# Performance work log

Measured on AMD Instinct MI355X. Metric: run time of the kernel, lower is better.

The kernel has to match this reference:

```python
import jax, jax.numpy as jnp
import numpy as np

B, S = 1024, 256
E, EU = 8, 1            # total experts, universal experts
ES = E - EU             # specialized experts
UW = 0.3                # universal_expert_weight
NSTEPS = 1001
COV = 512
H = 128
DATA_DIM = 2


def setup_inputs() -> dict:
    key = jax.random.key(0)
    ks = iter(jax.random.split(key, 64))

    def nrm(shape, s=0.02):
        return jax.random.normal(next(ks), shape, jnp.float32) * s

    inp = {
        "y_t": jax.random.normal(next(ks), (B, S, 1), jnp.float32),
        "y_0_hat": jax.random.normal(next(ks), (B, S, 1), jnp.float32),
        "cov_embedding": jax.random.normal(next(ks), (B, COV), jnp.float32),
        "t": jax.random.randint(next(ks), (B,), 0, NSTEPS),
    }
    for l, nin in zip((1, 2, 3), (DATA_DIM, H, H)):
        inp[f"l{l}_emb"] = jax.random.uniform(next(ks), (NSTEPS, H), jnp.float32)  # embed.weight.uniform_()
        inp[f"l{l}_W"] = nrm((E, nin, H))      # per-expert Linear weights
        inp[f"l{l}_b"] = jnp.zeros((E, H), jnp.float32)
        inp[f"l{l}_Wc"] = nrm((COV, H))        # cov_projection
        inp[f"l{l}_bc"] = jnp.zeros((H,), jnp.float32)
        inp[f"l{l}_Wr1"] = nrm((COV, COV // 2))  # specialized_router layer 1
        inp[f"l{l}_br1"] = jnp.zeros((COV // 2,), jnp.float32)
        inp[f"l{l}_Wr2"] = nrm((COV // 2, ES))   # specialized_router layer 2
        inp[f"l{l}_br2"] = jnp.zeros((ES,), jnp.float32)
    inp["W4"] = nrm((H, 1))
    inp["b4"] = jnp.zeros((1,), jnp.float32)
    return inp


def _moe_layer(x, t, cov, emb, W, b, Wc, bc, Wr1, br1, Wr2, br2):
    # x: [B,S,in]; t: [B] int; cov: [B,COV]
    gamma = emb[t][:, None, :]                                   # [B,1,H]
    hr = jax.nn.relu(cov @ Wr1 + br1)                            # router (dropout inactive in eval)
    rw = jax.nn.softmax(hr @ Wr2 + br2, axis=-1) * (1.0 - UW)    # [B,ES] specialized routing weights
    w = jnp.concatenate(
        [jnp.full((x.shape[0], EU), UW / EU, x.dtype), rw], axis=1
    )                                                            # [B,E] full routing weights
    # gamma factors out of the weighted sum over experts, so fuse expert GEMMs + weighting:
    mix = jnp.einsum('bsi,eio,be->bso', x, W, w) + jnp.einsum('be,eo->bo', w, b)[:, None, :]
    mix = gamma * mix
    cov_gamma = cov @ Wc + bc                                    # [B,H]
    mix = mix * (1.0 + cov_gamma[:, None, :])
    usage = rw.mean(axis=0)                                      # mean over batch
    load = jnp.mean((usage - 1.0 / ES) ** 2)                     # mse vs uniform
    return mix, load


def reference(y_t, y_0_hat, cov_embedding, t,
              l1_emb, l1_W, l1_b, l1_Wc, l1_bc, l1_Wr1, l1_br1, l1_Wr2, l1_br2,
              l2_emb, l2_W, l2_b, l2_Wc, l2_bc, l2_Wr1, l2_br1, l2_Wr2, l2_br2,
              l3_emb, l3_W, l3_b, l3_Wc, l3_bc, l3_Wr1, l3_br1, l3_Wr2, l3_br2,
              W4, b4):
    h = jnp.concatenate([y_t, y_0_hat], axis=-1)                 # cat_y_pred: [B,S,2]
    h, ld1 = _moe_layer(h, t, cov_embedding, l1_emb, l1_W, l1_b, l1_Wc, l1_bc, l1_Wr1, l1_br1, l1_Wr2, l1_br2)
    h = jax.nn.softplus(h)
    h, ld2 = _moe_layer(h, t, cov_embedding, l2_emb, l2_W, l2_b, l2_Wc, l2_bc, l2_Wr1, l2_br1, l2_Wr2, l2_br2)
    h = jax.nn.softplus(h)
    h, ld3 = _moe_layer(h, t, cov_embedding, l3_emb, l3_W, l3_b, l3_Wc, l3_bc, l3_Wr1, l3_br1, l3_Wr2, l3_br2)
    h = jax.nn.softplus(h)
    out = h @ W4 + b4                                            # [B,S,1] velocity
    return out, ld1 + ld2 + ld3
```

## Files before the change

### kernel.cpp

```cpp
#include <hip/hip_runtime.h>
#include <hip/hip_bf16.h>
#include <math.h>

#define B_    1024
#define S_    256
#define COV_  512
#define H_    128
#define E_    8
#define ES_   7

#define W_WS_OFF   0
#define COVG_OFF   24576
#define USAGE_OFF  417792

#define AT_STRIDE  136
#define WT_STRIDE  40

typedef __attribute__((ext_vector_type(8))) short bf16x8;
typedef __attribute__((ext_vector_type(4))) float f32x4;

__device__ __forceinline__ float softplus_f(float x) {
    return fmaxf(x, 0.0f) + __logf(1.0f + __expf(-fabsf(x)));
}

__device__ __forceinline__ unsigned pk2_bf16(float a, float b) {
    __hip_bfloat162 h = __float22bfloat162_rn(make_float2(a, b));
    return *reinterpret_cast<unsigned*>(&h);
}
__device__ __forceinline__ void split_pair(float a, float b, unsigned &hi, unsigned &lo) {
    hi = pk2_bf16(a, b);
    float ha = __uint_as_float(hi << 16);
    float hb = __uint_as_float(hi & 0xffff0000u);
    lo = pk2_bf16(a - ha, b - hb);
}

struct RouterArgs {
    const float* cov;
    const float* Wr1[3];
    const float* br1[3];
    const float* Wr2[3];
    const float* br2[3];
    const float* Wc[3];
    const float* bc[3];
    float* ws;
};

__global__ __launch_bounds__(768) void router_kernel(RouterArgs a) {
    const int l   = blockIdx.y;
    const int b0  = blockIdx.x * 8;
    const int tid = threadIdx.x;

    __shared__ float4 covs[8][COV_ / 4];
    __shared__ float  part[4][3072];
    __shared__ float  hr[8][256];
    __shared__ float  susage[ES_];
    if (tid < ES_) susage[tid] = 0.0f;

    for (int f = tid; f < 1024; f += 768) {
        const int bb = f >> 7, k4 = f & 127;
        covs[bb][k4] = ((const float4*)(a.cov + (size_t)(b0 + bb) * COV_))[k4];
    }
    __syncthreads();

    {
        const int cp = tid % 192;
        const int ks = tid / 192;
        const int c0 = cp * 2;
        const float* __restrict__ Wp; int rs;
        if (c0 < 256) { Wp = a.Wr1[l] + c0;         rs = 256; }
        else          { Wp = a.Wc[l]  + (c0 - 256); rs = 128; }

        float acc0[8], acc1[8];
        #pragma unroll
        for (int bb = 0; bb < 8; ++bb) { acc0[bb] = 0.f; acc1[bb] = 0.f; }

        const int k4beg = ks * 32, k4end = k4beg + 32;
        #pragma unroll 2
        for (int k4 = k4beg; k4 < k4end; ++k4) {
            float2 w0 = *(const float2*)(Wp + (size_t)(4 * k4 + 0) * rs);
            float2 w1 = *(const float2*)(Wp + (size_t)(4 * k4 + 1) * rs);
            float2 w2 = *(const float2*)(Wp + (size_t)(4 * k4 + 2) * rs);
            float2 w3 = *(const float2*)(Wp + (size_t)(4 * k4 + 3) * rs);
            #pragma unroll
            for (int bb = 0; bb < 8; ++bb) {
                float4 cv = covs[bb][k4];
                acc0[bb] = fmaf(cv.x, w0.x, acc0[bb]);
                acc1[bb] = fmaf(cv.x, w0.y, acc1[bb]);
                acc0[bb] = fmaf(cv.y, w1.x, acc0[bb]);
                acc1[bb] = fmaf(cv.y, w1.y, acc1[bb]);
                acc0[bb] = fmaf(cv.z, w2.x, acc0[bb]);
                acc1[bb] = fmaf(cv.z, w2.y, acc1[bb]);
                acc0[bb] = fmaf(cv.w, w3.x, acc0[bb]);
                acc1[bb] = fmaf(cv.w, w3.y, acc1[bb]);
            }
        }
        #pragma unroll
        for (int bb = 0; bb < 8; ++bb)
            *(float2*)&part[ks][bb * 384 + c0] = make_float2(acc0[bb], acc1[bb]);
    }
    __syncthreads();

    {
        const int p0 = tid * 4;
        float4 s = {0.f, 0.f, 0.f, 0.f};
        #pragma unroll
        for (int ks = 0; ks < 4; ++ks) {
            float4 v = *(const float4*)&part[ks][p0];
            s.x += v.x; s.y += v.y; s.z += v.z; s.w += v.w;
        }
        const int bb = p0 / 384;
        const int c  = p0 % 384;
        const float sv[4] = {s.x, s.y, s.z, s.w};
        if (c < 256) {
            #pragma unroll
            for (int q = 0; q < 4; ++q)
                hr[bb][c + q] = fmaxf(sv[q] + a.br1[l][c + q], 0.0f);
        } else {
            #pragma unroll
            for (int q = 0; q < 4; ++q)
                a.ws[COVG_OFF + (size_t)(l * B_ + b0 + bb) * H_ + (c - 256 + q)] = sv[q] + a.bc[l][c - 256 + q];
        }
    }
    __syncthreads();

    {
        const int wave = tid >> 6;
        const int lane = tid & 63;
        if (wave < 8) {
            const int bb = wave;
            const int o = lane >> 3;
            const int g = lane & 7;
            float p = 0.0f;
            if (o < ES_) {
                #pragma unroll
                for (int m = 0; m < 32; ++m) {
                    const int k = g * 32 + m;
                    p = fmaf(hr[bb][k], a.Wr2[l][k * ES_ + o], p);
                }
            }
            p += __shfl_xor(p, 1);
            p += __shfl_xor(p, 2);
            p += __shfl_xor(p, 4);
            const float lg = p + ((o < ES_) ? a.br2[l][o] : 0.0f);
            float v[ES_];
            #pragma unroll
            for (int oo = 0; oo < ES_; ++oo) v[oo] = __shfl(lg, oo * 8, 64);
            if (lane == 0) {
                const int b = b0 + bb;
                float mx = v[0];
                #pragma unroll
                for (int oo = 1; oo < ES_; ++oo) mx = fmaxf(mx, v[oo]);
                float ex[ES_]; float s = 0.0f;
                #pragma unroll
                for (int oo = 0; oo < ES_; ++oo) { ex[oo] = __expf(v[oo] - mx); s += ex[oo]; }
                const float inv = 0.7f / s;
                float* wout = a.ws + W_WS_OFF + (size_t)(l * B_ + b) * 8;
                wout[0] = 0.3f;
                #pragma unroll
                for (int oo = 0; oo < ES_; ++oo) {
                    const float rwv = ex[oo] * inv;
                    wout[1 + oo] = rwv;
                    atomicAdd(&susage[oo], rwv);
                }
            }
        }
    }
    __syncthreads();
    if (tid < ES_) atomicAdd(a.ws + USAGE_OFF + l * ES_ + tid, susage[tid]);
}

struct MainArgs {
    const float* y_t;
    const float* y0;
    const int*   t;
    const float* emb[3];
    const float* W1;
    const float* W2;
    const float* W3;
    const float* b_[3];
    const float* W4;
    const float* b4;
    float* ws;
    float* out;
};

__global__ __launch_bounds__(1024, 4) void main_kernel(MainArgs a) {
    __shared__ unsigned short Ahi[256 * AT_STRIDE];
    __shared__ unsigned short Alo[256 * AT_STRIDE];
    __shared__ unsigned short WtBuf[2][128 * WT_STRIDE];
    __shared__ float GPs[2][128];
    __shared__ float GPBs[2][128];
    __shared__ float W4s[128];

    const int tid  = threadIdx.x;
    const int b    = blockIdx.x;
    const int lane = tid & 63;
    const int w    = tid >> 6;
    const int wm   = w >> 1;
    const int wn   = w & 1;
    const int nl   = lane & 15;
    const int quad = lane >> 4;
    const int tb   = a.t[b];

    float* L1f = (float*)WtBuf;

    if (tid < 384) {
        const int l = tid >> 7, j = tid & 127;
        const float* wv = a.ws + W_WS_OFF + (size_t)(l * B_ + b) * 8;
        const float gamma = a.emb[l][tb * H_ + j];
        const float covg  = a.ws[COVG_OFF + (size_t)(l * B_ + b) * H_ + j];
        const float gp = gamma * (1.0f + covg);
        const float* bl = a.b_[l];
        float bm = 0.0f;
        #pragma unroll
        for (int e = 0; e < E_; ++e) bm = fmaf(wv[e], bl[e * H_ + j], bm);
        if (l == 0) {
            float s0 = 0.0f, s1 = 0.0f;
            #pragma unroll
            for (int e = 0; e < E_; ++e) {
                s0 = fmaf(wv[e], a.W1[e * 256 + j], s0);
                s1 = fmaf(wv[e], a.W1[e * 256 + 128 + j], s1);
            }
            L1f[j]       = gp * s0;
            L1f[128 + j] = gp * s1;
            L1f[256 + j] = gp * bm;
        } else {
            GPs[l - 1][j]  = gp;
            GPBs[l - 1][j] = gp * bm;
        }
    }
    if (tid < 128) W4s[tid] = a.W4[tid];
    __syncthreads();

    {
        const int tok = tid >> 2;
        const int jh  = (tid & 3) * 32;
        const float x0 = a.y_t[b * S_ + tok];
        const float x1 = a.y0[b * S_ + tok];
        #pragma unroll
        for (int g = 0; g < 4; ++g) {
            const int jb = jh + g * 8;
            unsigned hp[4], lp[4];
            #pragma unroll
            for (int p = 0; p < 4; ++p) {
                const int j0 = jb + 2 * p;
                float m0 = fmaf(x0, L1f[j0],     fmaf(x1, L1f[128 + j0],     L1f[256 + j0]));
                float m1 = fmaf(x0, L1f[j0 + 1], fmaf(x1, L1f[128 + j0 + 1], L1f[256 + j0 + 1]));
                split_pair(softplus_f(m0), softplus_f(m1), hp[p], lp[p]);
            }
            *(uint4*)&Ahi[tok * AT_STRIDE + jb] = make_uint4(hp[0], hp[1], hp[2], hp[3]);
            *(uint4*)&Alo[tok * AT_STRIDE + jb] = make_uint4(lp[0], lp[1], lp[2], lp[3]);
        }
    }

    const int bj  = tid & 127;
    const int bkg = tid >> 7;

    for (int L = 0; L < 2; ++L) {
        const float* __restrict__ Wg = L ? a.W3 : a.W2;
        const float* wv = a.ws + W_WS_OFF + (size_t)((L + 1) * B_ + b) * 8;
        float we[E_];
        #pragma unroll
        for (int e = 0; e < E_; ++e) we[e] = wv[e];

        f32x4 acc[2][4];
        #pragma unroll
        for (int mt = 0; mt < 2; ++mt)
            #pragma unroll
            for (int nt = 0; nt < 4; ++nt)
                acc[mt][nt] = (f32x4){0.f, 0.f, 0.f, 0.f};

        unsigned bh[2], blo_[2];
        auto build = [&](int kc) {
            float bacc[4] = {0.f, 0.f, 0.f, 0.f};
            const float* base = Wg + (size_t)(kc * 32 + bkg * 4) * H_ + bj;
            #pragma unroll
            for (int e = 0; e < E_; ++e) {
                const float* p = base + (size_t)e * (H_ * H_);
                const float wE = we[e];
                #pragma unroll
                for (int i = 0; i < 4; ++i)
                    bacc[i] = fmaf(wE, p[i * H_], bacc[i]);
            }
            split_pair(bacc[0], bacc[1], bh[0], blo_[0]);
            split_pair(bacc[2], bacc[3], bh[1], blo_[1]);
        };

        build(0);

        for (int kc = 0; kc < 4; ++kc) {
            __syncthreads();
            *(uint2*)&WtBuf[0][bj * WT_STRIDE + bkg * 4] = make_uint2(bh[0], bh[1]);
            *(uint2*)&WtBuf[1][bj * WT_STRIDE + bkg * 4] = make_uint2(blo_[0], blo_[1]);
            __syncthreads();

            const int ka = kc * 32 + quad * 8;
            bf16x8 Af[2], Al[2], Bf[4], Bl[4];
            #pragma unroll
            for (int mt = 0; mt < 2; ++mt) {
                const int row = (wm * 32 + mt * 16 + nl) * AT_STRIDE + ka;
                Af[mt] = *(const bf16x8*)&Ahi[row];
                Al[mt] = *(const bf16x8*)&Alo[row];
            }
            #pragma unroll
            for (int nt = 0; nt < 4; ++nt) {
                const int row = (wn * 64 + nt * 16 + nl) * WT_STRIDE + quad * 8;
                Bf[nt] = *(const bf16x8*)&WtBuf[0][row];
                Bl[nt] = *(const bf16x8*)&WtBuf[1][row];
            }
            #pragma unroll
            for (int mt = 0; mt < 2; ++mt)
                #pragma unroll
                for (int nt = 0; nt < 4; ++nt) {
                    acc[mt][nt] = __builtin_amdgcn_mfma_f32_16x16x32_bf16(Af[mt], Bf[nt], acc[mt][nt], 0, 0, 0);
                    acc[mt][nt] = __builtin_amdgcn_mfma_f32_16x16x32_bf16(Af[mt], Bl[nt], acc[mt][nt], 0, 0, 0);
                    acc[mt][nt] = __builtin_amdgcn_mfma_f32_16x16x32_bf16(Al[mt], Bf[nt], acc[mt][nt], 0, 0, 0);
                }

            if (kc < 3) build(kc + 1);
        }
        __syncthreads();

        if (L == 0) {
            #pragma unroll
            for (int nt = 0; nt < 4; ++nt) {
                const int n = wn * 64 + nt * 16 + nl;
                const float gp = GPs[0][n], gpb = GPBs[0][n];
                #pragma unroll
                for (int mt = 0; mt < 2; ++mt) {
                    const int tok0 = wm * 32 + mt * 16 + quad * 4;
                    #pragma unroll
                    for (int rp = 0; rp < 2; ++rp) {
                        const float h0 = softplus_f(fmaf(gp, acc[mt][nt][2 * rp],     gpb));
                        const float h1 = softplus_f(fmaf(gp, acc[mt][nt][2 * rp + 1], gpb));
                        unsigned hh, ll;
                        split_pair(h0, h1, hh, ll);
                        const int t0 = tok0 + 2 * rp;
                        Ahi[t0 * AT_STRIDE + n]       = (unsigned short)hh;
                        Ahi[(t0 + 1) * AT_STRIDE + n] = (unsigned short)(hh >> 16);
                        Alo[t0 * AT_STRIDE + n]       = (unsigned short)ll;
                        Alo[(t0 + 1) * AT_STRIDE + n] = (unsigned short)(ll >> 16);
                    }
                }
            }
        } else {
            float po[2][4];
            #pragma unroll
            for (int mt = 0; mt < 2; ++mt)
                #pragma unroll
                for (int r = 0; r < 4; ++r) po[mt][r] = 0.0f;
            #pragma unroll
            for (int nt = 0; nt < 4; ++nt) {
                const int n = wn * 64 + nt * 16 + nl;
                const float gp = GPs[1][n], gpb = GPBs[1][n], w4 = W4s[n];
                #pragma unroll
                for (int mt = 0; mt < 2; ++mt)
                    #pragma unroll
                    for (int r = 0; r < 4; ++r) {
                        const float h = softplus_f(fmaf(gp, acc[mt][nt][r], gpb));
                        po[mt][r] = fmaf(h, w4, po[mt][r]);
                    }
            }
            #pragma unroll
            for (int mt = 0; mt < 2; ++mt)
                #pragma unroll
                for (int r = 0; r < 4; ++r) {
                    po[mt][r] += __shfl_xor(po[mt][r], 1);
                    po[mt][r] += __shfl_xor(po[mt][r], 2);
                    po[mt][r] += __shfl_xor(po[mt][r], 4);
                    po[mt][r] += __shfl_xor(po[mt][r], 8);
                }
            float* pos = (float*)WtBuf;
            if (nl == 0) {
                #pragma unroll
                for (int mt = 0; mt < 2; ++mt)
                    #pragma unroll
                    for (int r = 0; r < 4; ++r)
                        pos[(wm * 32 + mt * 16 + quad * 4 + r) * 2 + wn] = po[mt][r];
            }
            __syncthreads();
            if (tid < 256)
                a.out[b * S_ + tid] = pos[2 * tid] + pos[2 * tid + 1] + a.b4[0];
        }
    }

    if (b == 0 && tid == 0) {
        float ld = 0.0f;
        for (int l = 0; l < 3; ++l)
            for (int o = 0; o < ES_; ++o) {
                float u = a.ws[USAGE_OFF + l * ES_ + o] * (1.0f / (float)B_);
                float d = u - (1.0f / (float)ES_);
                ld = fmaf(d, d, ld);
            }
        a.out[B_ * S_] = ld * (1.0f / (float)ES_);
    }
}

extern "C" void kernel_launch(void* const* d_in, const int* in_sizes, int n_in,
                              void* d_out, int out_size, void* d_ws, size_t ws_size,
                              hipStream_t stream) {
    (void)in_sizes; (void)n_in; (void)out_size; (void)ws_size;

    RouterArgs ra;
    ra.cov = (const float*)d_in[2];
    ra.ws  = (float*)d_ws;

    MainArgs ma;
    ma.y_t = (const float*)d_in[0];
    ma.y0  = (const float*)d_in[1];
    ma.t   = (const int*)d_in[3];
    for (int l = 0; l < 3; ++l) {
        const int base = 4 + l * 9;
        ma.emb[l] = (const float*)d_in[base + 0];
        ma.b_[l]  = (const float*)d_in[base + 2];
        ra.Wc[l]  = (const float*)d_in[base + 3];
        ra.bc[l]  = (const float*)d_in[base + 4];
        ra.Wr1[l] = (const float*)d_in[base + 5];
        ra.br1[l] = (const float*)d_in[base + 6];
        ra.Wr2[l] = (const float*)d_in[base + 7];
        ra.br2[l] = (const float*)d_in[base + 8];
    }
    ma.W1 = (const float*)d_in[4 + 0 * 9 + 1];
    ma.W2 = (const float*)d_in[4 + 1 * 9 + 1];
    ma.W3 = (const float*)d_in[4 + 2 * 9 + 1];
    ma.W4 = (const float*)d_in[31];
    ma.b4 = (const float*)d_in[32];
    ma.ws  = (float*)d_ws;
    ma.out = (float*)d_out;

    (void)hipMemsetAsync((char*)d_ws + USAGE_OFF * sizeof(float), 0, 24 * sizeof(float), stream);
    router_kernel<<<dim3(128, 3, 1), 768, 0, stream>>>(ra);
    main_kernel<<<dim3(1024, 1, 1), 1024, 0, stream>>>(ma);
}
```

Measured before the change: 291.4 us.

## Swizzle LDS layout, double-buffer weight tiles, drop memset and usage atomics

Replaces the padded LDS strides with XOR-swizzled layouts for the activation and combined-weight tiles, and double-buffers the weight tile so each k-chunk needs one barrier instead of two. Per-layer gamma, bias and W4 values now live in registers instead of shared memory. The router writes per-block usage partials rather than doing global atomics, so the memset launch goes away and block 0 reduces the partials at kernel start. The trade-off is higher register pressure under a 1024-thread launch bound, plus a serial 128-element reduction in block 0.

```diff
diff --git a/kernel.cpp b/kernel.cpp
--- a/kernel.cpp
+++ b/kernel.cpp
@@ -12,9 +12,6 @@
 #define W_WS_OFF   0
 #define COVG_OFF   24576
 #define USAGE_OFF  417792
-
-#define AT_STRIDE  136
-#define WT_STRIDE  40
 
 typedef __attribute__((ext_vector_type(8))) short bf16x8;
 typedef __attribute__((ext_vector_type(4))) float f32x4;
@@ -166,7 +163,8 @@
         }
     }
     __syncthreads();
-    if (tid < ES_) atomicAdd(a.ws + USAGE_OFF + l * ES_ + tid, susage[tid]);
+    if (tid < ES_)
+        a.ws[USAGE_OFF + (size_t)(l * 128 + blockIdx.x) * 8 + tid] = susage[tid];
 }
 
 struct MainArgs {
@@ -185,12 +183,9 @@
 };
 
 __global__ __launch_bounds__(1024, 4) void main_kernel(MainArgs a) {
-    __shared__ unsigned short Ahi[256 * AT_STRIDE];
-    __shared__ unsigned short Alo[256 * AT_STRIDE];
-    __shared__ unsigned short WtBuf[2][128 * WT_STRIDE];
-    __shared__ float GPs[2][128];
-    __shared__ float GPBs[2][128];
-    __shared__ float W4s[128];
+    __shared__ __align__(16) char smem[163840];
+    unsigned short* Ahi = (unsigned short*)smem;
+    unsigned short* Alo = (unsigned short*)(smem + 65536);
 
     const int tid  = threadIdx.x;
     const int b    = blockIdx.x;
@@ -202,44 +197,77 @@
     const int quad = lane >> 4;
     const int tb   = a.t[b];
 
-    float* L1f = (float*)WtBuf;
-
-    if (tid < 384) {
-        const int l = tid >> 7, j = tid & 127;
-        const float* wv = a.ws + W_WS_OFF + (size_t)(l * B_ + b) * 8;
-        const float gamma = a.emb[l][tb * H_ + j];
-        const float covg  = a.ws[COVG_OFF + (size_t)(l * B_ + b) * H_ + j];
-        const float gp = gamma * (1.0f + covg);
-        const float* bl = a.b_[l];
-        float bm = 0.0f;
-        #pragma unroll
-        for (int e = 0; e < E_; ++e) bm = fmaf(wv[e], bl[e * H_ + j], bm);
-        if (l == 0) {
-            float s0 = 0.0f, s1 = 0.0f;
-            #pragma unroll
-            for (int e = 0; e < E_; ++e) {
-                s0 = fmaf(wv[e], a.W1[e * 256 + j], s0);
-                s1 = fmaf(wv[e], a.W1[e * 256 + 128 + j], s1);
-            }
-            L1f[j]       = gp * s0;
-            L1f[128 + j] = gp * s1;
-            L1f[256 + j] = gp * bm;
-        } else {
-            GPs[l - 1][j]  = gp;
-            GPBs[l - 1][j] = gp * bm;
-        }
-    }
-    if (tid < 128) W4s[tid] = a.W4[tid];
+    if (b == 0 && tid < 64) {
+        float d2 = 0.0f;
+        if (tid < 21) {
+            const int l = tid / 7, o = tid % 7;
+            float s = 0.0f;
+            for (int bx = 0; bx < 128; ++bx)
+                s += a.ws[USAGE_OFF + (size_t)(l * 128 + bx) * 8 + o];
+            const float u = s * (1.0f / (float)B_);
+            const float d = u - (1.0f / (float)ES_);
+            d2 = d * d;
+        }
+        float tot = 0.0f;
+        #pragma unroll
+        for (int i = 0; i < 21; ++i) tot += __shfl(d2, i, 64);
+        if (tid == 0) a.out[B_ * S_] = tot * (1.0f / (float)ES_);
+    }
+
+    float wvL[2][E_];
+    #pragma unroll
+    for (int l = 0; l < 2; ++l) {
+        const float* wv = a.ws + W_WS_OFF + (size_t)((l + 1) * B_ + b) * 8;
+        #pragma unroll
+        for (int e = 0; e < E_; ++e) wvL[l][e] = wv[e];
+    }
+    float gpr[2][4], gpbr[2][4], w4r[4];
+    #pragma unroll
+    for (int l = 0; l < 2; ++l) {
+        const int li = l + 1;
+        #pragma unroll
+        for (int nt = 0; nt < 4; ++nt) {
+            const int n = wn * 64 + nt * 16 + nl;
+            const float covg  = a.ws[COVG_OFF + (size_t)(li * B_ + b) * H_ + n];
+            const float gamma = a.emb[li][tb * H_ + n];
+            const float gp = gamma * (1.0f + covg);
+            float bm = 0.0f;
+            #pragma unroll
+            for (int e = 0; e < E_; ++e) bm = fmaf(wvL[l][e], a.b_[li][e * H_ + n], bm);
+            gpr[l][nt]  = gp;
+            gpbr[l][nt] = gp * bm;
+            if (l == 1) w4r[nt] = a.W4[n];
+        }
+    }
+
+    float* L1f = (float*)(smem + 131072);
+    if (tid < 128) {
+        const int j = tid;
+        const float* wv = a.ws + W_WS_OFF + (size_t)b * 8;
+        float s0 = 0.f, s1 = 0.f, bm = 0.f;
+        #pragma unroll
+        for (int e = 0; e < E_; ++e) {
+            s0 = fmaf(wv[e], a.W1[e * 256 + j], s0);
+            s1 = fmaf(wv[e], a.W1[e * 256 + 128 + j], s1);
+            bm = fmaf(wv[e], a.b_[0][e * H_ + j], bm);
+        }
+        const float covg = a.ws[COVG_OFF + (size_t)b * H_ + j];
+        const float gp = a.emb[0][tb * H_ + j] * (1.0f + covg);
+        L1f[j]       = gp * s0;
+        L1f[128 + j] = gp * s1;
+        L1f[256 + j] = gp * bm;
+    }
     __syncthreads();
 
     {
         const int tok = tid >> 2;
-        const int jh  = (tid & 3) * 32;
         const float x0 = a.y_t[b * S_ + tok];
         const float x1 = a.y0[b * S_ + tok];
+        const int tsw = tok & 15;
         #pragma unroll
         for (int g = 0; g < 4; ++g) {
-            const int jb = jh + g * 8;
+            const int c  = (tid & 3) * 4 + g;
+            const int jb = c * 8;
             unsigned hp[4], lp[4];
             #pragma unroll
             for (int p = 0; p < 4; ++p) {
@@ -248,20 +276,19 @@
                 float m1 = fmaf(x0, L1f[j0 + 1], fmaf(x1, L1f[128 + j0 + 1], L1f[256 + j0 + 1]));
                 split_pair(softplus_f(m0), softplus_f(m1), hp[p], lp[p]);
             }
-            *(uint4*)&Ahi[tok * AT_STRIDE + jb] = make_uint4(hp[0], hp[1], hp[2], hp[3]);
-            *(uint4*)&Alo[tok * AT_STRIDE + jb] = make_uint4(lp[0], lp[1], lp[2], lp[3]);
-        }
-    }
-
-    const int bj  = tid & 127;
-    const int bkg = tid >> 7;
+            const int off = tok * 128 + ((c ^ tsw) << 3);
+            *(uint4*)&Ahi[off] = make_uint4(hp[0], hp[1], hp[2], hp[3]);
+            *(uint4*)&Alo[off] = make_uint4(lp[0], lp[1], lp[2], lp[3]);
+        }
+    }
+
+    const int bj   = tid & 127;
+    const int bkg  = tid >> 7;
+    const int bq   = bkg >> 1;
+    const int bwoff = bj * 32 + (((bq ^ ((bj >> 1) & 3)) << 3)) + (bkg & 1) * 4;
 
     for (int L = 0; L < 2; ++L) {
         const float* __restrict__ Wg = L ? a.W3 : a.W2;
-        const float* wv = a.ws + W_WS_OFF + (size_t)((L + 1) * B_ + b) * 8;
-        float we[E_];
-        #pragma unroll
-        for (int e = 0; e < E_; ++e) we[e] = wv[e];
 
         f32x4 acc[2][4];
         #pragma unroll
@@ -277,7 +304,7 @@
             #pragma unroll
             for (int e = 0; e < E_; ++e) {
                 const float* p = base + (size_t)e * (H_ * H_);
-                const float wE = we[e];
+                const float wE = wvL[L][e];
                 #pragma unroll
                 for (int i = 0; i < 4; ++i)
                     bacc[i] = fmaf(wE, p[i * H_], bacc[i]);
@@ -287,26 +314,33 @@
         };
 
         build(0);
+        __syncthreads();
+        {
+            unsigned short* wtH = (unsigned short*)(smem + 131072);
+            *(uint2*)&wtH[bwoff]        = make_uint2(bh[0], bh[1]);
+            *(uint2*)&wtH[4096 + bwoff] = make_uint2(blo_[0], blo_[1]);
+        }
+        __syncthreads();
 
         for (int kc = 0; kc < 4; ++kc) {
-            __syncthreads();
-            *(uint2*)&WtBuf[0][bj * WT_STRIDE + bkg * 4] = make_uint2(bh[0], bh[1]);
-            *(uint2*)&WtBuf[1][bj * WT_STRIDE + bkg * 4] = make_uint2(blo_[0], blo_[1]);
-            __syncthreads();
-
-            const int ka = kc * 32 + quad * 8;
+            unsigned short* wtH = (unsigned short*)(smem + 131072 + (kc & 1) * 16384);
+            unsigned short* wtL = wtH + 4096;
+            const int c = kc * 4 + quad;
+
             bf16x8 Af[2], Al[2], Bf[4], Bl[4];
             #pragma unroll
             for (int mt = 0; mt < 2; ++mt) {
-                const int row = (wm * 32 + mt * 16 + nl) * AT_STRIDE + ka;
-                Af[mt] = *(const bf16x8*)&Ahi[row];
-                Al[mt] = *(const bf16x8*)&Alo[row];
+                const int tok = wm * 32 + mt * 16 + nl;
+                const int off = tok * 128 + (((c ^ (tok & 15))) << 3);
+                Af[mt] = *(const bf16x8*)&Ahi[off];
+                Al[mt] = *(const bf16x8*)&Alo[off];
             }
             #pragma unroll
             for (int nt = 0; nt < 4; ++nt) {
-                const int row = (wn * 64 + nt * 16 + nl) * WT_STRIDE + quad * 8;
-                Bf[nt] = *(const bf16x8*)&WtBuf[0][row];
-                Bl[nt] = *(const bf16x8*)&WtBuf[1][row];
+                const int n = wn * 64 + nt * 16 + nl;
+                const int off = n * 32 + (((quad ^ ((n >> 1) & 3))) << 3);
+                Bf[nt] = *(const bf16x8*)&wtH[off];
+                Bl[nt] = *(const bf16x8*)&wtL[off];
             }
             #pragma unroll
             for (int mt = 0; mt < 2; ++mt)
@@ -317,15 +351,21 @@
                     acc[mt][nt] = __builtin_amdgcn_mfma_f32_16x16x32_bf16(Al[mt], Bf[nt], acc[mt][nt], 0, 0, 0);
                 }
 
-            if (kc < 3) build(kc + 1);
-        }
-        __syncthreads();
+            if (kc < 3) {
+                build(kc + 1);
+                unsigned short* dH = (unsigned short*)(smem + 131072 + ((kc + 1) & 1) * 16384);
+                *(uint2*)&dH[bwoff]        = make_uint2(bh[0], bh[1]);
+                *(uint2*)&dH[4096 + bwoff] = make_uint2(blo_[0], blo_[1]);
+            }
+            __syncthreads();
+        }
 
         if (L == 0) {
             #pragma unroll
             for (int nt = 0; nt < 4; ++nt) {
                 const int n = wn * 64 + nt * 16 + nl;
-                const float gp = GPs[0][n], gpb = GPBs[0][n];
+                const float gp = gpr[0][nt], gpb = gpbr[0][nt];
+                const int nc = n >> 3, np = n & 7;
                 #pragma unroll
                 for (int mt = 0; mt < 2; ++mt) {
                     const int tok0 = wm * 32 + mt * 16 + quad * 4;
@@ -336,10 +376,12 @@
                         unsigned hh, ll;
                         split_pair(h0, h1, hh, ll);
                         const int t0 = tok0 + 2 * rp;
-                        Ahi[t0 * AT_STRIDE + n]       = (unsigned short)hh;
-                        Ahi[(t0 + 1) * AT_STRIDE + n] = (unsigned short)(hh >> 16);
-                        Alo[t0 * AT_STRIDE + n]       = (unsigned short)ll;
-                        Alo[(t0 + 1) * AT_STRIDE + n] = (unsigned short)(ll >> 16);
+                        const int o0 = t0 * 128       + (((nc ^ (t0 & 15)))       << 3) + np;
+                        const int o1 = (t0 + 1) * 128 + (((nc ^ ((t0 + 1) & 15))) << 3) + np;
+                        Ahi[o0] = (unsigned short)hh;
+                        Ahi[o1] = (unsigned short)(hh >> 16);
+                        Alo[o0] = (unsigned short)ll;
+                        Alo[o1] = (unsigned short)(ll >> 16);
                     }
                 }
             }
@@ -351,8 +393,7 @@
                 for (int r = 0; r < 4; ++r) po[mt][r] = 0.0f;
             #pragma unroll
             for (int nt = 0; nt < 4; ++nt) {
-                const int n = wn * 64 + nt * 16 + nl;
-                const float gp = GPs[1][n], gpb = GPBs[1][n], w4 = W4s[n];
+                const float gp = gpr[1][nt], gpb = gpbr[1][nt], w4 = w4r[nt];
                 #pragma unroll
                 for (int mt = 0; mt < 2; ++mt)
                     #pragma unroll
@@ -370,7 +411,7 @@
                     po[mt][r] += __shfl_xor(po[mt][r], 4);
                     po[mt][r] += __shfl_xor(po[mt][r], 8);
                 }
-            float* pos = (float*)WtBuf;
+            float* pos = (float*)(smem + 131072);
             if (nl == 0) {
                 #pragma unroll
                 for (int mt = 0; mt < 2; ++mt)
@@ -382,17 +423,6 @@
             if (tid < 256)
                 a.out[b * S_ + tid] = pos[2 * tid] + pos[2 * tid + 1] + a.b4[0];
         }
-    }
-
-    if (b == 0 && tid == 0) {
-        float ld = 0.0f;
-        for (int l = 0; l < 3; ++l)
-            for (int o = 0; o < ES_; ++o) {
-                float u = a.ws[USAGE_OFF + l * ES_ + o] * (1.0f / (float)B_);
-                float d = u - (1.0f / (float)ES_);
-                ld = fmaf(d, d, ld);
-            }
-        a.out[B_ * S_] = ld * (1.0f / (float)ES_);
     }
 }
 
@@ -428,7 +458,6 @@
     ma.ws  = (float*)d_ws;
     ma.out = (float*)d_out;
 
-    (void)hipMemsetAsync((char*)d_ws + USAGE_OFF * sizeof(float), 0, 24 * sizeof(float), stream);
     router_kernel<<<dim3(128, 3, 1), 768, 0, stream>>>(ra);
     main_kernel<<<dim3(1024, 1, 1), 1024, 0, stream>>>(ma);
 }
```

Result: slower. 430.3 us (+47.7%).
